# Kernel optimization log

Hardware: AMD Instinct MI355X
Metric: run time of the kernel (lower is better)

Reference implementation:

```python
import jax, jax.numpy as jnp
import numpy as np

ALPHA = 0.0005
TAU = 0.2


def setup_inputs() -> dict:
    key = jax.random.key(0)
    k1, k2, k3 = jax.random.split(key, 3)
    output = jax.random.normal(k1, (8192, 1000), dtype=jnp.float32)
    target = jax.random.normal(k2, (8192, 1000), dtype=jnp.float32)
    conv_w = jax.random.normal(k3, (256, 256, 128, 3), dtype=jnp.float32)
    return {"output": output, "target": target, "conv_w": conv_w}


def reference(output, target, conv_w):
    # base loss (nn.MSELoss with default 'mean' reduction)
    loss = jnp.mean((output - target) ** 2)

    # Diversity regularizer: pairwise cosine similarity between slices
    # conv_w[:, :, i, :] along dim 2 ('filters' = size(2) in the original).
    F = conv_w.shape[2]
    # V: [F, D] with D = out_ch * in_ch * kw
    V = jnp.transpose(conv_w, (2, 0, 1, 3)).reshape(F, -1)
    norms = jnp.linalg.norm(V, axis=1)                      # [F]
    G = (V @ V.T) / (norms[:, None] * norms[None, :])       # [F, F] cosine Gram

    # keep entries with tau < sim <= 1 and i != j
    offdiag = ~jnp.eye(F, dtype=bool)
    mask = (G > TAU) & (G <= 1.0) & offdiag
    reg = jnp.sum(jnp.where(mask, G, jnp.zeros((), dtype=G.dtype)))

    return loss + ALPHA * reg
```

## Files before the change

### kernel.cpp

```cpp
#include <hip/hip_runtime.h>
#include <hip/hip_bf16.h>


typedef __attribute__((ext_vector_type(8))) short bf16x8;
typedef __attribute__((ext_vector_type(4))) float f32x4;

#define ALPHA 0.0005f
#define TAU 0.2f

#define FDIM 128
#define TSTRIDE 52
#define GRAM_NBLK 512
#define NMSE 1536
#define CHUNK_F4 3072
#define GRAM_ELEMS 16384
#define NPAIRQ 8192
#define MSE_N4 2048000

__device__ __forceinline__ unsigned int pack_bf2(float lo, float hi) {
    union { float f; unsigned int u; } a, b;
    a.f = lo; b.f = hi;
    unsigned int al = (a.u + 0x7fffu + ((a.u >> 16) & 1u)) >> 16;
    unsigned int bh = (b.u + 0x7fffu + ((b.u >> 16) & 1u)) & 0xffff0000u;
    return (al & 0xffffu) | bh;
}

__device__ __forceinline__ void mfmaph(const unsigned short* __restrict__ tu,
                                       int wave, int colr, int hi8,
                                       f32x4 (&acc0)[8], f32x4 (&acc1)[8]) {
#pragma unroll
    for (int ks = 0; ks < 3; ++ks) {
        const int koff = ks * 32 + hi8;
        bf16x8 a0 = *reinterpret_cast<const bf16x8*>(
            &tu[(wave * 32 + colr) * (TSTRIDE * 2) + koff]);
        bf16x8 a1 = *reinterpret_cast<const bf16x8*>(
            &tu[(wave * 32 + 16 + colr) * (TSTRIDE * 2) + koff]);
#pragma unroll
        for (int cc = 0; cc < 8; ++cc) {
            bf16x8 b = *reinterpret_cast<const bf16x8*>(
                &tu[(cc * 16 + colr) * (TSTRIDE * 2) + koff]);
            acc0[cc] = __builtin_amdgcn_mfma_f32_16x16x32_bf16(a0, b, acc0[cc], 0, 0, 0);
            acc1[cc] = __builtin_amdgcn_mfma_f32_16x16x32_bf16(a1, b, acc1[cc], 0, 0, 0);
        }
    }
}

__global__ void __launch_bounds__(256, 4) fused_kernel(
        const float* __restrict__ o, const float* __restrict__ t,
        const float* __restrict__ conv,
        float* __restrict__ mse_part, unsigned int* __restrict__ pp) {
    __shared__ unsigned int tile[FDIM * TSTRIDE];
    __shared__ float red[4];
    const int tid = threadIdx.x;
    const int lane = tid & 63;
    const int wave = tid >> 6;

    if (blockIdx.x >= GRAM_NBLK) {
        const int mb = blockIdx.x - GRAM_NBLK;
        const int gid = mb * 256 + tid;
        const f32x4* o4 = reinterpret_cast<const f32x4*>(o);
        const f32x4* t4 = reinterpret_cast<const f32x4*>(t);
        float s = 0.f;
        for (int i = gid; i < MSE_N4; i += NMSE * 256) {
            f32x4 a = o4[i], b = t4[i];
            f32x4 d = a - b;
            s += d[0]*d[0] + d[1]*d[1] + d[2]*d[2] + d[3]*d[3];
        }
        for (int off = 32; off; off >>= 1) s += __shfl_down(s, off);
        if (lane == 0) red[wave] = s;
        __syncthreads();
        if (tid == 0) mse_part[mb] = red[0] + red[1] + red[2] + red[3];
        return;
    }

    const int p = tid >> 4;
    const int q = tid & 15;
    const int colr = lane & 15;
    const int hi8 = (lane >> 4) * 8;
    const unsigned short* tileu = reinterpret_cast<const unsigned short*>(tile);

    f32x4 acc0[8], acc1[8];
#pragma unroll
    for (int cc = 0; cc < 8; ++cc) { acc0[cc] = (f32x4)0.f; acc1[cc] = (f32x4)0.f; }

    const f32x4* src4 = reinterpret_cast<const f32x4*>(conv);
    const size_t cb = (size_t)blockIdx.x * (4 * CHUNK_F4) + (2 * p) * 96 + q;

    for (int c = 0; c < 4; ++c) {
        __syncthreads();
#pragma unroll
        for (int it = 0; it < 6; ++it) {
            const f32x4 v0 = src4[cb + c * CHUNK_F4 + 16 * it];
            const f32x4 v1 = src4[cb + c * CHUNK_F4 + 96 + 16 * it];
            const int off4 = q + 16 * it;
#pragma unroll
            for (int u = 0; u < 4; ++u) {
                const int idx = off4 * 4 + u;
                const int f = idx / 3;
                const int k = idx - 3 * f;
                tile[f * TSTRIDE + k * 16 + p] = pack_bf2(v0[u], v1[u]);
            }
        }
        __syncthreads();
        mfmaph(tileu, wave, colr, hi8, acc0, acc1);
    }

    unsigned int* myp = pp + (size_t)blockIdx.x * NPAIRQ;
    const int rsub = (lane >> 4) << 2;
#pragma unroll
    for (int cc = 0; cc < 8; ++cc) {
        const int col = cc * 16 + colr;
#pragma unroll
        for (int j = 0; j < 4; ++j) {
            const int pr = wave * 16 + rsub + j;
            myp[pr * FDIM + col] = pack_bf2(acc0[cc][j], acc1[cc][j]);
        }
    }
}

__global__ void __launch_bounds__(256) reduce_kernel(
        const unsigned int* __restrict__ pp, float* __restrict__ gram) {
    __shared__ float red[16][16][2];
    const int tid = threadIdx.x;
    const int u = tid & 15;
    const int s = tid >> 4;
    const int qq = blockIdx.x * 16 + u;
    float lo = 0.f, hi = 0.f;
#pragma unroll 8
    for (int b = s * 32; b < s * 32 + 32; ++b) {
        const unsigned int v = pp[(size_t)b * NPAIRQ + qq];
        lo += __uint_as_float(v << 16);
        hi += __uint_as_float(v & 0xffff0000u);
    }
    red[s][u][0] = lo; red[s][u][1] = hi;
    __syncthreads();
    if (tid < 32) {
        const int u2 = tid >> 1, h = tid & 1;
        float x = 0.f;
#pragma unroll
        for (int s2 = 0; s2 < 16; ++s2) x += red[s2][u2][h];
        gram[(blockIdx.x * 16 + u2) * 2 + h] = x;
    }
}

__global__ void __launch_bounds__(256) finalize_kernel(
        const float* __restrict__ gram, const float* __restrict__ mse_part,
        float* __restrict__ out) {
    __shared__ float rn[FDIM];
    __shared__ float redS[4], redM[4];
    const int tid = threadIdx.x;
    if (tid < FDIM) {
        const int row = tid;
        const int pr = (row >> 5) * 16 + (row & 15);
        const int h = (row >> 4) & 1;
        rn[row] = rsqrtf(gram[(pr * FDIM + row) * 2 + h]);
    }
    __syncthreads();
    float s = 0.f;
    for (int i = tid; i < GRAM_ELEMS; i += 256) {
        const int h = i & 1;
        const int qq = i >> 1;
        const int col = qq & 127;
        const int pr = qq >> 7;
        const int row = (pr >> 4) * 32 + (pr & 15) + (h << 4);
        const float gv = gram[i] * rn[row] * rn[col];
        if (row != col && gv > TAU && gv <= 1.0f) s += gv;
    }
    float m = 0.f;
#pragma unroll 6
    for (int j = 0; j < 6; ++j) m += mse_part[tid * 6 + j];
    for (int off = 32; off; off >>= 1) {
        s += __shfl_down(s, off);
        m += __shfl_down(m, off);
    }
    if ((tid & 63) == 0) { redS[tid >> 6] = s; redM[tid >> 6] = m; }
    __syncthreads();
    if (tid == 0)
        out[0] = (redM[0] + redM[1] + redM[2] + redM[3]) * (1.0f / 8192000.0f) +
                 ALPHA * (redS[0] + redS[1] + redS[2] + redS[3]);
}

extern "C" void kernel_launch(void* const* d_in, const int* in_sizes, int n_in,
                              void* d_out, int out_size, void* d_ws, size_t ws_size,
                              hipStream_t stream) {
    const float* output = (const float*)d_in[0];
    const float* target = (const float*)d_in[1];
    const float* conv   = (const float*)d_in[2];
    float* out = (float*)d_out;

    float* wsf       = (float*)d_ws;
    float* mse_part  = wsf;
    float* gram      = wsf + NMSE;
    unsigned int* pp = (unsigned int*)(wsf + NMSE + GRAM_ELEMS);
    (void)ws_size;

    fused_kernel<<<GRAM_NBLK + NMSE, 256, 0, stream>>>(output, target, conv,
                                                       mse_part, pp);
    reduce_kernel<<<NPAIRQ / 16, 256, 0, stream>>>(pp, gram);
    finalize_kernel<<<1, 256, 0, stream>>>(gram, mse_part, out);
}
```

Before: 57.77 us.

## Split fused kernel into separate Gram and MSE kernels with 512-thread Gram blocks

Splits the fused MSE+Gram kernel into two launches: a 512-thread Gram kernel where each of eight waves computes one 16-row strip, and a standalone MSE kernel with 2048 blocks. Global loads in the Gram tile fill are batched before the bf16 packing, and the partial-product layout and finalize indexing change to match. The intent is fewer accumulator registers per thread for better occupancy and less imbalance between the two workloads. The cost is an extra kernel launch and no overlap between the MSE and Gram work.

```diff
diff --git a/kernel.cpp b/kernel.cpp
--- a/kernel.cpp
+++ b/kernel.cpp
@@ -11,11 +11,11 @@
 #define FDIM 128
 #define TSTRIDE 52
 #define GRAM_NBLK 512
-#define NMSE 1536
 #define CHUNK_F4 3072
 #define GRAM_ELEMS 16384
 #define NPAIRQ 8192
 #define MSE_N4 2048000
+#define MSE_NBLK 2048
 
 __device__ __forceinline__ unsigned int pack_bf2(float lo, float hi) {
     union { float f; unsigned int u; } a, b;
@@ -25,95 +25,85 @@
     return (al & 0xffffu) | bh;
 }
 
-__device__ __forceinline__ void mfmaph(const unsigned short* __restrict__ tu,
-                                       int wave, int colr, int hi8,
-                                       f32x4 (&acc0)[8], f32x4 (&acc1)[8]) {
-#pragma unroll
-    for (int ks = 0; ks < 3; ++ks) {
-        const int koff = ks * 32 + hi8;
-        bf16x8 a0 = *reinterpret_cast<const bf16x8*>(
-            &tu[(wave * 32 + colr) * (TSTRIDE * 2) + koff]);
-        bf16x8 a1 = *reinterpret_cast<const bf16x8*>(
-            &tu[(wave * 32 + 16 + colr) * (TSTRIDE * 2) + koff]);
-#pragma unroll
-        for (int cc = 0; cc < 8; ++cc) {
-            bf16x8 b = *reinterpret_cast<const bf16x8*>(
-                &tu[(cc * 16 + colr) * (TSTRIDE * 2) + koff]);
-            acc0[cc] = __builtin_amdgcn_mfma_f32_16x16x32_bf16(a0, b, acc0[cc], 0, 0, 0);
-            acc1[cc] = __builtin_amdgcn_mfma_f32_16x16x32_bf16(a1, b, acc1[cc], 0, 0, 0);
-        }
+__global__ void __launch_bounds__(256) mse_kernel(
+        const float* __restrict__ o, const float* __restrict__ t,
+        float* __restrict__ mse_part) {
+    __shared__ float red[4];
+    const int tid = threadIdx.x;
+    const float4* o4 = reinterpret_cast<const float4*>(o);
+    const float4* t4 = reinterpret_cast<const float4*>(t);
+    float s = 0.f;
+    for (int i = blockIdx.x * 256 + tid; i < MSE_N4; i += MSE_NBLK * 256) {
+        float4 a = o4[i], b = t4[i];
+        float dx = a.x - b.x, dy = a.y - b.y, dz = a.z - b.z, dw = a.w - b.w;
+        s += dx * dx + dy * dy + dz * dz + dw * dw;
     }
+    for (int off = 32; off; off >>= 1) s += __shfl_down(s, off);
+    if ((tid & 63) == 0) red[tid >> 6] = s;
+    __syncthreads();
+    if (tid == 0) mse_part[blockIdx.x] = red[0] + red[1] + red[2] + red[3];
 }
 
-__global__ void __launch_bounds__(256, 4) fused_kernel(
-        const float* __restrict__ o, const float* __restrict__ t,
-        const float* __restrict__ conv,
-        float* __restrict__ mse_part, unsigned int* __restrict__ pp) {
+__global__ void __launch_bounds__(512, 6) gram_kernel(
+        const float* __restrict__ conv, unsigned int* __restrict__ pp) {
     __shared__ unsigned int tile[FDIM * TSTRIDE];
-    __shared__ float red[4];
     const int tid = threadIdx.x;
     const int lane = tid & 63;
     const int wave = tid >> 6;
-
-    if (blockIdx.x >= GRAM_NBLK) {
-        const int mb = blockIdx.x - GRAM_NBLK;
-        const int gid = mb * 256 + tid;
-        const f32x4* o4 = reinterpret_cast<const f32x4*>(o);
-        const f32x4* t4 = reinterpret_cast<const f32x4*>(t);
-        float s = 0.f;
-        for (int i = gid; i < MSE_N4; i += NMSE * 256) {
-            f32x4 a = o4[i], b = t4[i];
-            f32x4 d = a - b;
-            s += d[0]*d[0] + d[1]*d[1] + d[2]*d[2] + d[3]*d[3];
-        }
-        for (int off = 32; off; off >>= 1) s += __shfl_down(s, off);
-        if (lane == 0) red[wave] = s;
-        __syncthreads();
-        if (tid == 0) mse_part[mb] = red[0] + red[1] + red[2] + red[3];
-        return;
-    }
-
-    const int p = tid >> 4;
-    const int q = tid & 15;
+    const int sp = tid >> 5;
+    const int q = tid & 31;
     const int colr = lane & 15;
     const int hi8 = (lane >> 4) * 8;
     const unsigned short* tileu = reinterpret_cast<const unsigned short*>(tile);
 
-    f32x4 acc0[8], acc1[8];
+    f32x4 acc0[8];
 #pragma unroll
-    for (int cc = 0; cc < 8; ++cc) { acc0[cc] = (f32x4)0.f; acc1[cc] = (f32x4)0.f; }
+    for (int cc = 0; cc < 8; ++cc) acc0[cc] = (f32x4)0.f;
 
     const f32x4* src4 = reinterpret_cast<const f32x4*>(conv);
-    const size_t cb = (size_t)blockIdx.x * (4 * CHUNK_F4) + (2 * p) * 96 + q;
+    const size_t cb = (size_t)blockIdx.x * (4 * CHUNK_F4) + sp * 192 + q;
 
     for (int c = 0; c < 4; ++c) {
         __syncthreads();
+        f32x4 V0[3], V1[3];
 #pragma unroll
-        for (int it = 0; it < 6; ++it) {
-            const f32x4 v0 = src4[cb + c * CHUNK_F4 + 16 * it];
-            const f32x4 v1 = src4[cb + c * CHUNK_F4 + 96 + 16 * it];
-            const int off4 = q + 16 * it;
+        for (int it = 0; it < 3; ++it) {
+            V0[it] = src4[cb + c * CHUNK_F4 + 32 * it];
+            V1[it] = src4[cb + c * CHUNK_F4 + 96 + 32 * it];
+        }
+#pragma unroll
+        for (int it = 0; it < 3; ++it)
 #pragma unroll
             for (int u = 0; u < 4; ++u) {
-                const int idx = off4 * 4 + u;
+                const int idx = (q + 32 * it) * 4 + u;
                 const int f = idx / 3;
                 const int k = idx - 3 * f;
-                tile[f * TSTRIDE + k * 16 + p] = pack_bf2(v0[u], v1[u]);
+                tile[f * TSTRIDE + k * 16 + sp] = pack_bf2(V0[it][u], V1[it][u]);
+            }
+        __syncthreads();
+#pragma unroll
+        for (int ks = 0; ks < 3; ++ks) {
+            const int koff = ks * 32 + hi8;
+            bf16x8 a0 = *reinterpret_cast<const bf16x8*>(
+                &tileu[(wave * 16 + colr) * (TSTRIDE * 2) + koff]);
+#pragma unroll
+            for (int cc = 0; cc < 8; ++cc) {
+                bf16x8 b = *reinterpret_cast<const bf16x8*>(
+                    &tileu[(cc * 16 + colr) * (TSTRIDE * 2) + koff]);
+                acc0[cc] = __builtin_amdgcn_mfma_f32_16x16x32_bf16(a0, b, acc0[cc], 0, 0, 0);
             }
         }
-        __syncthreads();
-        mfmaph(tileu, wave, colr, hi8, acc0, acc1);
     }
 
     unsigned int* myp = pp + (size_t)blockIdx.x * NPAIRQ;
     const int rsub = (lane >> 4) << 2;
 #pragma unroll
-    for (int cc = 0; cc < 8; ++cc) {
-        const int col = cc * 16 + colr;
+    for (int cc = 0; cc < 4; ++cc) {
+        const int clo = cc * 16 + colr;
 #pragma unroll
         for (int j = 0; j < 4; ++j) {
-            const int pr = wave * 16 + rsub + j;
-            myp[pr * FDIM + col] = pack_bf2(acc0[cc][j], acc1[cc][j]);
+            const int row = wave * 16 + rsub + j;
+            myp[row * 64 + clo] = pack_bf2(acc0[cc][j], acc0[cc + 4][j]);
         }
     }
 }
@@ -150,25 +140,22 @@
     __shared__ float redS[4], redM[4];
     const int tid = threadIdx.x;
     if (tid < FDIM) {
-        const int row = tid;
-        const int pr = (row >> 5) * 16 + (row & 15);
-        const int h = (row >> 4) & 1;
-        rn[row] = rsqrtf(gram[(pr * FDIM + row) * 2 + h]);
+        const int r = tid;
+        rn[r] = rsqrtf(gram[(r * 64 + (r & 63)) * 2 + (r >> 6)]);
     }
     __syncthreads();
     float s = 0.f;
     for (int i = tid; i < GRAM_ELEMS; i += 256) {
         const int h = i & 1;
         const int qq = i >> 1;
-        const int col = qq & 127;
-        const int pr = qq >> 7;
-        const int row = (pr >> 4) * 32 + (pr & 15) + (h << 4);
+        const int row = qq >> 6;
+        const int col = (qq & 63) | (h << 6);
         const float gv = gram[i] * rn[row] * rn[col];
         if (row != col && gv > TAU && gv <= 1.0f) s += gv;
     }
     float m = 0.f;
-#pragma unroll 6
-    for (int j = 0; j < 6; ++j) m += mse_part[tid * 6 + j];
+#pragma unroll 8
+    for (int j = 0; j < 8; ++j) m += mse_part[tid * 8 + j];
     for (int off = 32; off; off >>= 1) {
         s += __shfl_down(s, off);
         m += __shfl_down(m, off);
@@ -190,12 +177,12 @@
 
     float* wsf       = (float*)d_ws;
     float* mse_part  = wsf;
-    float* gram      = wsf + NMSE;
-    unsigned int* pp = (unsigned int*)(wsf + NMSE + GRAM_ELEMS);
+    float* gram      = wsf + MSE_NBLK;
+    unsigned int* pp = (unsigned int*)(wsf + MSE_NBLK + GRAM_ELEMS);
     (void)ws_size;
 
-    fused_kernel<<<GRAM_NBLK + NMSE, 256, 0, stream>>>(output, target, conv,
-                                                       mse_part, pp);
+    gram_kernel<<<GRAM_NBLK, 512, 0, stream>>>(conv, pp);
+    mse_kernel<<<MSE_NBLK, 256, 0, stream>>>(output, target, mse_part);
     reduce_kernel<<<NPAIRQ / 16, 256, 0, stream>>>(pp, gram);
     finalize_kernel<<<1, 256, 0, stream>>>(gram, mse_part, out);
 }
```

Result: slower. 66.44 us (+15.0%).

## Split Gram work across twice as many blocks with a smaller padded K tile

Applied to the files above, without the earlier changes.

The Gram partial-product blocks double from 512 to 1024, and each block now stages a 48-wide K slice per chunk instead of 96. The slice is zero-padded to 64 so it maps onto two bf16 MFMA k-steps. The MSE block count rises to 2048 with an unrolled loop, and launch bounds allow 5 blocks per SM. The goal is more parallelism and occupancy from smaller LDS tiles. The cost is twice as many bf16 partial Gram matrices (32 MB) to write and reduce, plus MFMA work spent on the zero padding.

```diff
diff --git a/kernel.cpp b/kernel.cpp
--- a/kernel.cpp
+++ b/kernel.cpp
@@ -9,12 +9,11 @@
 #define TAU 0.2f
 
 #define FDIM 128
-#define TSTRIDE 52
-#define GRAM_NBLK 512
-#define NMSE 1536
-#define CHUNK_F4 3072
+#define TS 36
+#define NGRAM 1024
+#define NMSE 2048
+#define NPAIRQ 8192
 #define GRAM_ELEMS 16384
-#define NPAIRQ 8192
 #define MSE_N4 2048000
 
 __device__ __forceinline__ unsigned int pack_bf2(float lo, float hi) {
@@ -25,42 +24,23 @@
     return (al & 0xffffu) | bh;
 }
 
-__device__ __forceinline__ void mfmaph(const unsigned short* __restrict__ tu,
-                                       int wave, int colr, int hi8,
-                                       f32x4 (&acc0)[8], f32x4 (&acc1)[8]) {
-#pragma unroll
-    for (int ks = 0; ks < 3; ++ks) {
-        const int koff = ks * 32 + hi8;
-        bf16x8 a0 = *reinterpret_cast<const bf16x8*>(
-            &tu[(wave * 32 + colr) * (TSTRIDE * 2) + koff]);
-        bf16x8 a1 = *reinterpret_cast<const bf16x8*>(
-            &tu[(wave * 32 + 16 + colr) * (TSTRIDE * 2) + koff]);
-#pragma unroll
-        for (int cc = 0; cc < 8; ++cc) {
-            bf16x8 b = *reinterpret_cast<const bf16x8*>(
-                &tu[(cc * 16 + colr) * (TSTRIDE * 2) + koff]);
-            acc0[cc] = __builtin_amdgcn_mfma_f32_16x16x32_bf16(a0, b, acc0[cc], 0, 0, 0);
-            acc1[cc] = __builtin_amdgcn_mfma_f32_16x16x32_bf16(a1, b, acc1[cc], 0, 0, 0);
-        }
-    }
-}
-
-__global__ void __launch_bounds__(256, 4) fused_kernel(
+__global__ void __launch_bounds__(256, 5) fused_kernel(
         const float* __restrict__ o, const float* __restrict__ t,
         const float* __restrict__ conv,
         float* __restrict__ mse_part, unsigned int* __restrict__ pp) {
-    __shared__ unsigned int tile[FDIM * TSTRIDE];
+    __shared__ unsigned int tile[FDIM * TS];
     __shared__ float red[4];
     const int tid = threadIdx.x;
     const int lane = tid & 63;
     const int wave = tid >> 6;
 
-    if (blockIdx.x >= GRAM_NBLK) {
-        const int mb = blockIdx.x - GRAM_NBLK;
+    if (blockIdx.x >= NGRAM) {
+        const int mb = blockIdx.x - NGRAM;
         const int gid = mb * 256 + tid;
         const f32x4* o4 = reinterpret_cast<const f32x4*>(o);
         const f32x4* t4 = reinterpret_cast<const f32x4*>(t);
         float s = 0.f;
+#pragma unroll 4
         for (int i = gid; i < MSE_N4; i += NMSE * 256) {
             f32x4 a = o4[i], b = t4[i];
             f32x4 d = a - b;
@@ -73,36 +53,55 @@
         return;
     }
 
-    const int p = tid >> 4;
-    const int q = tid & 15;
+    const int p = tid >> 5;
+    const int q = tid & 31;
     const int colr = lane & 15;
     const int hi8 = (lane >> 4) * 8;
     const unsigned short* tileu = reinterpret_cast<const unsigned short*>(tile);
 
+    for (int z = tid; z < FDIM * 8; z += 256)
+        tile[(z >> 3) * TS + 24 + (z & 7)] = 0;
+
     f32x4 acc0[8], acc1[8];
 #pragma unroll
     for (int cc = 0; cc < 8; ++cc) { acc0[cc] = (f32x4)0.f; acc1[cc] = (f32x4)0.f; }
 
     const f32x4* src4 = reinterpret_cast<const f32x4*>(conv);
-    const size_t cb = (size_t)blockIdx.x * (4 * CHUNK_F4) + (2 * p) * 96 + q;
+    const size_t cb = (size_t)blockIdx.x * 6144 + (2 * p) * 96 + q;
 
     for (int c = 0; c < 4; ++c) {
         __syncthreads();
-#pragma unroll
-        for (int it = 0; it < 6; ++it) {
-            const f32x4 v0 = src4[cb + c * CHUNK_F4 + 16 * it];
-            const f32x4 v1 = src4[cb + c * CHUNK_F4 + 96 + 16 * it];
-            const int off4 = q + 16 * it;
+        f32x4 V0[3], V1[3];
+#pragma unroll
+        for (int jj = 0; jj < 3; ++jj) {
+            V0[jj] = src4[cb + c * 1536 + 32 * jj];
+            V1[jj] = src4[cb + c * 1536 + 96 + 32 * jj];
+        }
+#pragma unroll
+        for (int jj = 0; jj < 3; ++jj)
 #pragma unroll
             for (int u = 0; u < 4; ++u) {
-                const int idx = off4 * 4 + u;
+                const int idx = (q + 32 * jj) * 4 + u;
                 const int f = idx / 3;
                 const int k = idx - 3 * f;
-                tile[f * TSTRIDE + k * 16 + p] = pack_bf2(v0[u], v1[u]);
+                tile[f * TS + k * 8 + p] = pack_bf2(V0[jj][u], V1[jj][u]);
             }
-        }
         __syncthreads();
-        mfmaph(tileu, wave, colr, hi8, acc0, acc1);
+#pragma unroll
+        for (int ks = 0; ks < 2; ++ks) {
+            const int koff = ks * 32 + hi8;
+            bf16x8 a0 = *reinterpret_cast<const bf16x8*>(
+                &tileu[(wave * 32 + colr) * (TS * 2) + koff]);
+            bf16x8 a1 = *reinterpret_cast<const bf16x8*>(
+                &tileu[(wave * 32 + 16 + colr) * (TS * 2) + koff]);
+#pragma unroll
+            for (int cc = 0; cc < 8; ++cc) {
+                bf16x8 b = *reinterpret_cast<const bf16x8*>(
+                    &tileu[(cc * 16 + colr) * (TS * 2) + koff]);
+                acc0[cc] = __builtin_amdgcn_mfma_f32_16x16x32_bf16(a0, b, acc0[cc], 0, 0, 0);
+                acc1[cc] = __builtin_amdgcn_mfma_f32_16x16x32_bf16(a1, b, acc1[cc], 0, 0, 0);
+            }
+        }
     }
 
     unsigned int* myp = pp + (size_t)blockIdx.x * NPAIRQ;
@@ -127,7 +126,7 @@
     const int qq = blockIdx.x * 16 + u;
     float lo = 0.f, hi = 0.f;
 #pragma unroll 8
-    for (int b = s * 32; b < s * 32 + 32; ++b) {
+    for (int b = s * 64; b < s * 64 + 64; ++b) {
         const unsigned int v = pp[(size_t)b * NPAIRQ + qq];
         lo += __uint_as_float(v << 16);
         hi += __uint_as_float(v & 0xffff0000u);
@@ -167,8 +166,8 @@
         if (row != col && gv > TAU && gv <= 1.0f) s += gv;
     }
     float m = 0.f;
-#pragma unroll 6
-    for (int j = 0; j < 6; ++j) m += mse_part[tid * 6 + j];
+#pragma unroll 8
+    for (int j = 0; j < 8; ++j) m += mse_part[tid * 8 + j];
     for (int off = 32; off; off >>= 1) {
         s += __shfl_down(s, off);
         m += __shfl_down(m, off);
@@ -194,8 +193,8 @@
     unsigned int* pp = (unsigned int*)(wsf + NMSE + GRAM_ELEMS);
     (void)ws_size;
 
-    fused_kernel<<<GRAM_NBLK + NMSE, 256, 0, stream>>>(output, target, conv,
-                                                       mse_part, pp);
+    fused_kernel<<<NGRAM + NMSE, 256, 0, stream>>>(output, target, conv,
+                                                   mse_part, pp);
     reduce_kernel<<<NPAIRQ / 16, 256, 0, stream>>>(pp, gram);
     finalize_kernel<<<1, 256, 0, stream>>>(gram, mse_part, out);
 }
```

After: 79.38 us. +37.4%, slower.
